# Kernel tuning notes

Hardware: AMD Instinct MI355X
Metric: run time of the kernel (lower is better)

The kernel has to match this reference:

```python
import jax, jax.numpy as jnp
import numpy as np

TASK_NUM = 100000
WORKER_NUM = 500
FEATURE_SIZE = 512
CLASS_NUM = 10
ANSWER_NUM = 1000000
HIDDEN = 128
NUM_NODES = TASK_NUM + WORKER_NUM


def setup_inputs() -> dict:
    key = jax.random.key(0)
    ks = jax.random.split(key, 10)
    task_ids = jax.random.randint(ks[0], (ANSWER_NUM,), 0, TASK_NUM, dtype=jnp.int32)
    worker_ids = jax.random.randint(ks[1], (ANSWER_NUM,), 0, WORKER_NUM, dtype=jnp.int32)
    label_ids = jax.random.randint(ks[2], (ANSWER_NUM,), 0, CLASS_NUM, dtype=jnp.int32)
    answers = jnp.stack([task_ids, worker_ids, label_ids], axis=1)  # [A,3]
    return {
        "task_feature": jax.random.normal(ks[3], (TASK_NUM, FEATURE_SIZE), jnp.float32),
        "answers": answers,
        "worker_feature": jax.random.normal(ks[4], (WORKER_NUM, HIDDEN), jnp.float32),
        "W_efc": jax.random.normal(ks[5], (FEATURE_SIZE, HIDDEN), jnp.float32) * 0.05,
        "b_efc": jnp.zeros((HIDDEN,), jnp.float32),
        "W_mean": jax.random.normal(ks[6], (HIDDEN, CLASS_NUM), jnp.float32) * 0.05,
        "b_mean": jnp.zeros((CLASS_NUM,), jnp.float32),
        "W_log_std": jax.random.normal(ks[7], (HIDDEN, CLASS_NUM), jnp.float32) * 0.05,
        "b_log_std": jnp.zeros((CLASS_NUM,), jnp.float32),
        "eps": jax.random.normal(ks[8], (NUM_NODES, CLASS_NUM), jnp.float32),
    }


def _gcn_edges(task_ids, worker_ids):
    # Bipartite edges doubled to be symmetric, plus self-loops (renorm trick).
    row0 = task_ids
    col0 = worker_ids + TASK_NUM
    self_idx = jnp.arange(NUM_NODES, dtype=jnp.int32)
    row = jnp.concatenate([row0, col0, self_idx])
    col = jnp.concatenate([col0, row0, self_idx])
    deg = jax.ops.segment_sum(jnp.ones_like(row, dtype=jnp.float32), row,
                              num_segments=NUM_NODES)
    dinv = jax.lax.rsqrt(deg)  # deg >= 1 thanks to self-loops
    w = dinv[row] * dinv[col]  # [E]
    return row, col, w, row0, col0


def _gcn(x, kernel, bias, row, col, w):
    h = x @ kernel                                   # [N, C]
    msg = h[col] * w[:, None]                        # gather + scale
    return jax.ops.segment_sum(msg, row, num_segments=NUM_NODES) + bias


def reference(task_feature, answers, worker_feature, W_efc, b_efc,
              W_mean, b_mean, W_log_std, b_log_std, eps):
    row, col, w, row0, col0 = _gcn_edges(answers[:, 0], answers[:, 1])
    tf_h = jax.nn.relu(task_feature @ W_efc + b_efc)           # [T, 128]
    x = jnp.concatenate([tf_h, worker_feature], axis=0)        # [N, 128]
    mean = _gcn(x, W_mean, b_mean, row, col, w)                # [N, C]
    log_std = _gcn(x, W_log_std, b_log_std, row, col, w)       # [N, C]
    z = mean + (eps * 0.01) * jnp.exp(log_std)                 # reparam, stddev 0.01
    crowd_out = z[row0] * z[col0]                              # [A, C]
    return crowd_out, mean, log_std
```

## Files before the change

kernel.cpp:

```cpp
#include <hip/hip_runtime.h>

#define T_NUM   100000
#define W_NUM   500
#define N_NODES 100500
#define A_NUM   1000000
#define FEAT    512
#define HID     128
#define CLS     10

#define CSR_STRIDE  40
#define CSRT_STRIDE 2432
#define BM          64
#define HPAD        136
#define NRANGE      8
#define TRNG        (T_NUM / NRANGE)

typedef short bf16x8 __attribute__((ext_vector_type(8)));
typedef float f32x4  __attribute__((ext_vector_type(4)));

__device__ __forceinline__ unsigned short f2bf(float f) {
    unsigned int u = __float_as_uint(f);
    unsigned int r = (u + 0x7FFFu + ((u >> 16) & 1u)) >> 16;
    return (unsigned short)r;
}

__global__ void k_build(const int* __restrict__ answers, int* __restrict__ cnt,
                        int* __restrict__ wcur,
                        unsigned short* __restrict__ csrW, int* __restrict__ csrT) {
    const int r      = blockIdx.x & (NRANGE - 1);
    const int grpblk = gridDim.x >> 3;
    const int gtid   = (blockIdx.x >> 3) * blockDim.x + threadIdx.x;
    const int gstr   = grpblk * blockDim.x;
    const int tlo    = r * TRNG, thi = tlo + TRNG;

    for (int a = gtid; a < A_NUM; a += gstr) {
        int t = answers[a * 3 + 0];
        int w = answers[a * 3 + 1];
        if (t >= tlo && t < thi) {
            int p = atomicAdd(&cnt[t], 1);
            if (p < CSR_STRIDE) csrW[(size_t)t * CSR_STRIDE + p] = (unsigned short)w;
        }
        if ((w * NRANGE) / W_NUM == r) {
            int q = atomicAdd(&wcur[w * 16], 1);
            if (q < CSRT_STRIDE) csrT[(size_t)w * CSRT_STRIDE + q] = t;
        }
    }
}

__global__ void k_prepw(const float* __restrict__ W, unsigned short* __restrict__ Wt,
                        unsigned short* __restrict__ B2t,
                        const float* __restrict__ WF,
                        const float* __restrict__ Wm, const float* __restrict__ Wl,
                        const int* __restrict__ wcur,
                        float* __restrict__ g) {
    int bid = blockIdx.x;
    if (bid < HID) {
        int c = bid;
        for (int k = threadIdx.x; k < FEAT; k += blockDim.x)
            Wt[(size_t)c * FEAT + k] = f2bf(W[(size_t)k * HID + c]);
    } else if (bid == HID) {
        for (int i = threadIdx.x; i < 32 * HID; i += blockDim.x) {
            int c = i / HID, k = i % HID;
            float v = 0.f;
            if (c < 10)                 v = Wm[k * CLS + c];
            else if (c >= 16 && c < 26) v = Wl[k * CLS + (c - 16)];
            B2t[i] = f2bf(v);
        }
    } else {
        int idx = (bid - HID - 1) * blockDim.x + threadIdx.x;
        if (idx >= W_NUM * 20) return;
        int w = idx / 20, oc = idx % 20;
        const float* Wc = (oc < 10) ? (Wm + oc) : (Wl + (oc - 10));
        const float* x  = WF + (size_t)w * HID;
        float s = 0.f;
        #pragma unroll 8
        for (int k = 0; k < HID; k++) s = fmaf(x[k], Wc[k * CLS], s);
        float gi = rsqrtf((float)(wcur[w * 16] + 1)) * s;
        g[(size_t)(T_NUM + w) * 20 + oc] = gi;
    }
}

__global__ __launch_bounds__(256, 7) void k_gemm_mfma(
        const float* __restrict__ A, const unsigned short* __restrict__ Wt,
        const float* __restrict__ bias, const unsigned short* __restrict__ B2t,
        const int* __restrict__ cnt, float* __restrict__ g) {
    __shared__ __align__(16) char smem[17408];

    const int tid  = threadIdx.x;
    const int lane = tid & 63;
    const int wv   = tid >> 6;
    const int l15  = lane & 15;
    const int lkg  = lane >> 4;
    const int row  = blockIdx.x * BM + wv * 16 + l15;
    const int rowc = row < T_NUM ? row : T_NUM - 1;
    const float* aptr = A + (size_t)rowc * FEAT + lkg * 8;

    const int scol  = tid >> 1;
    const int shalf = tid & 1;
    const int sswz  = (scol & 7) << 4;
    const int sb0   = (scol * 64 + shalf * 32) ^ sswz;
    const int sb1   = (scol * 64 + shalf * 32 + 16) ^ sswz;
    const unsigned short* sptr = Wt + (size_t)scol * FEAT + shalf * 16;

    const int rswz = (l15 & 7) << 4;

    f32x4 acc[8];
    #pragma unroll
    for (int nt = 0; nt < 8; nt++) acc[nt] = (f32x4){0.f, 0.f, 0.f, 0.f};

    union LU { int4 i; bf16x8 h; };
    union PK { unsigned short u[8]; bf16x8 h; };

    float4 ca0 = *(const float4*)(aptr);
    float4 ca1 = *(const float4*)(aptr + 4);
    *(int4*)(smem + sb0) = *(const int4*)(sptr);
    *(int4*)(smem + sb1) = *(const int4*)(sptr + 8);
    __syncthreads();

    for (int ks = 0; ks < 16; ks++) {
        const int k0 = ks * 32;
        float4 na0, na1;
        if (ks < 15) {
            na0 = *(const float4*)(aptr + k0 + 32);
            na1 = *(const float4*)(aptr + k0 + 36);
            char* nb = smem + (((ks + 1) & 1) << 13);
            *(int4*)(nb + sb0) = *(const int4*)(sptr + k0 + 32);
            *(int4*)(nb + sb1) = *(const int4*)(sptr + k0 + 40);
        }
        PK pk;
        pk.u[0] = f2bf(ca0.x); pk.u[1] = f2bf(ca0.y);
        pk.u[2] = f2bf(ca0.z); pk.u[3] = f2bf(ca0.w);
        pk.u[4] = f2bf(ca1.x); pk.u[5] = f2bf(ca1.y);
        pk.u[6] = f2bf(ca1.z); pk.u[7] = f2bf(ca1.w);
        const char* bb = smem + ((ks & 1) << 13);
        #pragma unroll
        for (int nt = 0; nt < 8; nt++) {
            const int boff = ((nt * 16 + l15) * 64 + lkg * 16) ^ rswz;
            LU bu; bu.i = *(const int4*)(bb + boff);
            acc[nt] = __builtin_amdgcn_mfma_f32_16x16x32_bf16(pk.h, bu.h, acc[nt], 0, 0, 0);
        }
        ca0 = na0; ca1 = na1;
        __syncthreads();
    }

    unsigned short* hw = (unsigned short*)smem + wv * 16 * HPAD;
    #pragma unroll
    for (int nt = 0; nt < 8; nt++) {
        float bv = bias[nt * 16 + l15];
        #pragma unroll
        for (int r = 0; r < 4; r++) {
            float h = fmaxf(acc[nt][r] + bv, 0.f);
            hw[(lkg * 4 + r) * HPAD + nt * 16 + l15] = f2bf(h);
        }
    }

    f32x4 acc2[2];
    acc2[0] = (f32x4){0.f, 0.f, 0.f, 0.f};
    acc2[1] = (f32x4){0.f, 0.f, 0.f, 0.f};
    #pragma unroll
    for (int s = 0; s < 4; s++) {
        LU a2;
        a2.i = *(const int4*)(hw + l15 * HPAD + s * 32 + lkg * 8);
        #pragma unroll
        for (int j = 0; j < 2; j++) {
            LU b2;
            b2.i = *(const int4*)(B2t + (size_t)(j * 16 + l15) * HID + s * 32 + lkg * 8);
            acc2[j] = __builtin_amdgcn_mfma_f32_16x16x32_bf16(a2.h, b2.h, acc2[j], 0, 0, 0);
        }
    }

    if (l15 < 10) {
        #pragma unroll
        for (int r = 0; r < 4; r++) {
            int node = blockIdx.x * BM + wv * 16 + lkg * 4 + r;
            if (node < T_NUM) {
                float di = rsqrtf((float)(cnt[node] + 1));
                g[(size_t)node * 20 + l15]      = di * acc2[0][r];
                g[(size_t)node * 20 + 10 + l15] = di * acc2[1][r];
            }
        }
    }
}

__global__ __launch_bounds__(256) void k_wacc(
        const int* __restrict__ csrT, const int* __restrict__ wcur,
        const float* __restrict__ g,
        const float* __restrict__ b_mean, const float* __restrict__ b_ls,
        const float* __restrict__ eps,
        float* __restrict__ out_mean, float* __restrict__ out_ls,
        float* __restrict__ z) {
    const int w    = blockIdx.x;
    const int tid  = threadIdx.x;
    const int lane = tid & 63;
    const int wv   = tid >> 6;

    int len = wcur[w * 16];
    int lim = len < CSRT_STRIDE ? len : CSRT_STRIDE;
    const int* lst = csrT + (size_t)w * CSRT_STRIDE;

    float a[20];
    #pragma unroll
    for (int c = 0; c < 20; c++) a[c] = 0.f;

    for (int e = tid; e < lim; e += 256) {
        int t = lst[e];
        const float4* gr = (const float4*)(g + (size_t)t * 20);
        float4 v0 = gr[0], v1 = gr[1], v2 = gr[2], v3 = gr[3], v4 = gr[4];
        a[0] += v0.x; a[1] += v0.y; a[2] += v0.z; a[3] += v0.w;
        a[4] += v1.x; a[5] += v1.y; a[6] += v1.z; a[7] += v1.w;
        a[8] += v2.x; a[9] += v2.y; a[10] += v2.z; a[11] += v2.w;
        a[12] += v3.x; a[13] += v3.y; a[14] += v3.z; a[15] += v3.w;
        a[16] += v4.x; a[17] += v4.y; a[18] += v4.z; a[19] += v4.w;
    }

    #pragma unroll
    for (int off = 32; off; off >>= 1) {
        #pragma unroll
        for (int c = 0; c < 20; c++) a[c] += __shfl_down(a[c], off, 64);
    }

    __shared__ float wpart[4][20];
    __shared__ float fin[20];
    if (lane == 0) {
        #pragma unroll
        for (int c = 0; c < 20; c++) wpart[wv][c] = a[c];
    }
    __syncthreads();

    const int node = T_NUM + w;
    if (tid < 20) {
        float s = wpart[0][tid] + wpart[1][tid] + wpart[2][tid] + wpart[3][tid];
        float di = rsqrtf((float)(len + 1));
        float gv = g[(size_t)node * 20 + tid];
        if (tid < 10) {
            float m = fmaf(di, s + gv, b_mean[tid]);
            out_mean[(size_t)node * CLS + tid] = m;
            fin[tid] = m;
        } else {
            int c = tid - 10;
            float l = fmaf(di, s + gv, b_ls[c]);
            out_ls[(size_t)node * CLS + c] = l;
            fin[tid] = l;
        }
    }
    __syncthreads();
    if (tid < 10) {
        float m = fin[tid], l = fin[tid + 10];
        z[(size_t)node * CLS + tid] =
            fmaf(eps[(size_t)node * CLS + tid] * 0.01f, expf(l), m);
    }
}

__global__ __launch_bounds__(256) void k_gather_task(
        const int* __restrict__ cnt, const unsigned short* __restrict__ csrW,
        const float* __restrict__ g,
        const float* __restrict__ b_mean, const float* __restrict__ b_ls,
        const float* __restrict__ eps,
        float* __restrict__ out_mean, float* __restrict__ out_ls,
        float* __restrict__ z) {
    __shared__ float gw[W_NUM * 21];
    for (int i = threadIdx.x; i < W_NUM * 20; i += blockDim.x)
        gw[(i / 20) * 21 + (i % 20)] = g[(size_t)T_NUM * 20 + i];
    __syncthreads();

    int t = blockIdx.x * blockDim.x + threadIdx.x;
    if (t >= T_NUM) return;

    int len = cnt[t];
    int lim = len < CSR_STRIDE ? len : CSR_STRIDE;
    const unsigned short* lst = csrW + (size_t)t * CSR_STRIDE;
    float am[10], al[10];
    #pragma unroll
    for (int c = 0; c < 10; c++) { am[c] = 0.f; al[c] = 0.f; }

    for (int e = 0; e < lim; e++) {
        const float* gg = &gw[lst[e] * 21];
        #pragma unroll
        for (int c = 0; c < 10; c++) {
            am[c] += gg[c];
            al[c] += gg[10 + c];
        }
    }

    float di = rsqrtf((float)(len + 1));
    union { float4 v[5]; float f[20]; } grow;
    const float4* gr = (const float4*)(g + (size_t)t * 20);
    #pragma unroll
    for (int c = 0; c < 5; c++) grow.v[c] = gr[c];

    const float2* ep2 = (const float2*)(eps + (size_t)t * CLS);
    float2* om2 = (float2*)(out_mean + (size_t)t * CLS);
    float2* ol2 = (float2*)(out_ls + (size_t)t * CLS);
    float2* z2  = (float2*)(z + (size_t)t * CLS);
    #pragma unroll
    for (int c = 0; c < 5; c++) {
        float2 ev = ep2[c];
        float m0 = fmaf(di, am[2 * c] + grow.f[2 * c], b_mean[2 * c]);
        float m1 = fmaf(di, am[2 * c + 1] + grow.f[2 * c + 1], b_mean[2 * c + 1]);
        float l0 = fmaf(di, al[2 * c] + grow.f[10 + 2 * c], b_ls[2 * c]);
        float l1 = fmaf(di, al[2 * c + 1] + grow.f[10 + 2 * c + 1], b_ls[2 * c + 1]);
        om2[c] = make_float2(m0, m1);
        ol2[c] = make_float2(l0, l1);
        z2[c]  = make_float2(fmaf(ev.x * 0.01f, expf(l0), m0),
                             fmaf(ev.y * 0.01f, expf(l1), m1));
    }
}

__global__ void k_crowd(const int* __restrict__ answers, const float* __restrict__ z,
                        float* __restrict__ out) {
    int a = blockIdx.x * blockDim.x + threadIdx.x;
    if (a >= A_NUM) return;
    int t = answers[a * 3 + 0];
    int w = answers[a * 3 + 1];
    const float2* zt = (const float2*)(z + (size_t)t * CLS);
    const float2* zw = (const float2*)(z + (size_t)(T_NUM + w) * CLS);
    float2* o = (float2*)(out + (size_t)a * CLS);
    #pragma unroll
    for (int c = 0; c < 5; c++) {
        float2 x = zt[c], y = zw[c];
        o[c] = make_float2(x.x * y.x, x.y * y.y);
    }
}

extern "C" void kernel_launch(void* const* d_in, const int* in_sizes, int n_in,
                              void* d_out, int out_size, void* d_ws, size_t ws_size,
                              hipStream_t stream) {
    const float* task_feature   = (const float*)d_in[0];
    const int*   answers        = (const int*)d_in[1];
    const float* worker_feature = (const float*)d_in[2];
    const float* W_efc          = (const float*)d_in[3];
    const float* b_efc          = (const float*)d_in[4];
    const float* W_mean         = (const float*)d_in[5];
    const float* b_mean         = (const float*)d_in[6];
    const float* W_ls           = (const float*)d_in[7];
    const float* b_ls           = (const float*)d_in[8];
    const float* eps            = (const float*)d_in[9];

    float* out       = (float*)d_out;
    float* out_crowd = out;
    float* out_mean  = out + (size_t)A_NUM * CLS;
    float* out_ls    = out_mean + (size_t)N_NODES * CLS;

    char* ws = (char*)d_ws;
    int* cnt              = (int*)ws;
    int* wcur             = (int*)(ws + 402432);
    unsigned short* csrW  = (unsigned short*)(ws + 434432);
    unsigned short* Wt    = (unsigned short*)(ws + 8434432);
    unsigned short* B2t   = (unsigned short*)(ws + 8565504);
    int* csrT             = (int*)(ws + 8573696);
    float* g              = (float*)(ws + 13437696);
    float* z              = (float*)(ws + 21477696);

    hipMemsetAsync(ws, 0, 434432, stream);

    k_build<<<2048, 256, 0, stream>>>(answers, cnt, wcur, csrW, csrT);
    k_prepw<<<HID + 1 + (W_NUM * 20 + 255) / 256, 256, 0, stream>>>(
        W_efc, Wt, B2t, worker_feature, W_mean, W_ls, wcur, g);
    k_gemm_mfma<<<(T_NUM + BM - 1) / BM, 256, 0, stream>>>(
        task_feature, Wt, b_efc, B2t, cnt, g);
    k_wacc<<<W_NUM, 256, 0, stream>>>(csrT, wcur, g, b_mean, b_ls, eps,
                                      out_mean, out_ls, z);
    k_gather_task<<<(T_NUM + 255) / 256, 256, 0, stream>>>(
        cnt, csrW, g, b_mean, b_ls, eps, out_mean, out_ls, z);
    k_crowd<<<(A_NUM + 255) / 256, 256, 0, stream>>>(answers, z, out_crowd);
}
```

Measured before the change: 240.1 us.

## Partition CSR build by hardware XCC id with per-XCC dynamic chunk queues

The CSR build kernel now reads the XCC id from a hardware register and uses it to pick which task/worker range a block owns, so atomics on each range stay within one XCC's L2. Blocks pull chunks of answers from a per-range atomic ticket counter instead of using a static grid-stride split. This aims to cut cross-die atomic traffic and balance load. It relies on blocks being spread evenly across the 8 XCCs, and the worker split changes to w>>6. It also adds a ticket array to the workspace and to the memset.

```diff
diff --git a/kernel.cpp b/kernel.cpp
--- a/kernel.cpp
+++ b/kernel.cpp
@@ -14,6 +14,8 @@
 #define HPAD        136
 #define NRANGE      8
 #define TRNG        (T_NUM / NRANGE)
+#define CHUNK       2048
+#define NCHUNK      ((A_NUM + CHUNK - 1) / CHUNK)
 
 typedef short bf16x8 __attribute__((ext_vector_type(8)));
 typedef float f32x4  __attribute__((ext_vector_type(4)));
@@ -24,26 +26,36 @@
     return (unsigned short)r;
 }
 
-__global__ void k_build(const int* __restrict__ answers, int* __restrict__ cnt,
-                        int* __restrict__ wcur,
-                        unsigned short* __restrict__ csrW, int* __restrict__ csrT) {
-    const int r      = blockIdx.x & (NRANGE - 1);
-    const int grpblk = gridDim.x >> 3;
-    const int gtid   = (blockIdx.x >> 3) * blockDim.x + threadIdx.x;
-    const int gstr   = grpblk * blockDim.x;
-    const int tlo    = r * TRNG, thi = tlo + TRNG;
-
-    for (int a = gtid; a < A_NUM; a += gstr) {
-        int t = answers[a * 3 + 0];
-        int w = answers[a * 3 + 1];
-        if (t >= tlo && t < thi) {
-            int p = atomicAdd(&cnt[t], 1);
-            if (p < CSR_STRIDE) csrW[(size_t)t * CSR_STRIDE + p] = (unsigned short)w;
-        }
-        if ((w * NRANGE) / W_NUM == r) {
-            int q = atomicAdd(&wcur[w * 16], 1);
-            if (q < CSRT_STRIDE) csrT[(size_t)w * CSRT_STRIDE + q] = t;
-        }
+__global__ __launch_bounds__(256) void k_build(
+        const int* __restrict__ answers, int* __restrict__ cnt,
+        int* __restrict__ wcur, int* __restrict__ tick,
+        unsigned short* __restrict__ csrW, int* __restrict__ csrT) {
+    __shared__ int s_chunk;
+    int xcc;
+    asm volatile("s_getreg_b32 %0, hwreg(HW_REG_XCC_ID)" : "=s"(xcc));
+    const int r   = xcc & (NRANGE - 1);
+    const int tlo = r * TRNG, thi = tlo + TRNG;
+
+    for (;;) {
+        if (threadIdx.x == 0) s_chunk = atomicAdd(&tick[r * 16], 1);
+        __syncthreads();
+        const int c = s_chunk;
+        if (c >= NCHUNK) break;
+        const int base = c * CHUNK;
+        const int end  = (base + CHUNK < A_NUM) ? base + CHUNK : A_NUM;
+        for (int a = base + threadIdx.x; a < end; a += 256) {
+            int t = answers[a * 3 + 0];
+            int w = answers[a * 3 + 1];
+            if (t >= tlo && t < thi) {
+                int p = atomicAdd(&cnt[t], 1);
+                if (p < CSR_STRIDE) csrW[(size_t)t * CSR_STRIDE + p] = (unsigned short)w;
+            }
+            if ((w >> 6) == r) {
+                int q = atomicAdd(&wcur[w * 16], 1);
+                if (q < CSRT_STRIDE) csrT[(size_t)w * CSRT_STRIDE + q] = t;
+            }
+        }
+        __syncthreads();
     }
 }
 
@@ -344,16 +356,17 @@
     char* ws = (char*)d_ws;
     int* cnt              = (int*)ws;
     int* wcur             = (int*)(ws + 402432);
-    unsigned short* csrW  = (unsigned short*)(ws + 434432);
-    unsigned short* Wt    = (unsigned short*)(ws + 8434432);
-    unsigned short* B2t   = (unsigned short*)(ws + 8565504);
-    int* csrT             = (int*)(ws + 8573696);
-    float* g              = (float*)(ws + 13437696);
-    float* z              = (float*)(ws + 21477696);
-
-    hipMemsetAsync(ws, 0, 434432, stream);
-
-    k_build<<<2048, 256, 0, stream>>>(answers, cnt, wcur, csrW, csrT);
+    int* tick             = (int*)(ws + 434432);
+    unsigned short* csrW  = (unsigned short*)(ws + 434944);
+    unsigned short* Wt    = (unsigned short*)(ws + 8434944);
+    unsigned short* B2t   = (unsigned short*)(ws + 8566016);
+    int* csrT             = (int*)(ws + 8574208);
+    float* g              = (float*)(ws + 13438208);
+    float* z              = (float*)(ws + 21478208);
+
+    hipMemsetAsync(ws, 0, 434944, stream);
+
+    k_build<<<2048, 256, 0, stream>>>(answers, cnt, wcur, tick, csrW, csrT);
     k_prepw<<<HID + 1 + (W_NUM * 20 + 255) / 256, 256, 0, stream>>>(
         W_efc, Wt, B2t, worker_feature, W_mean, W_ls, wcur, g);
     k_gemm_mfma<<<(T_NUM + BM - 1) / BM, 256, 0, stream>>>(
```

Result: no change. 243.5 us (+1.4%).
